# Kernel optimization log

Hardware: AMD Instinct MI355X
Metric: run time of the kernel (lower is better)

The kernel has to match this reference:

```python
import jax, jax.numpy as jnp
import numpy as np

B, T, D, M = 8, 4096, 64, 1024  # batch, frames, embedding_dim, codebook size


def setup_inputs() -> dict:
    key = jax.random.key(0)
    k1, k2, k3 = jax.random.split(key, 3)
    x = jax.random.normal(k1, (B, D, T), dtype=jnp.float32)          # (B, channels=D, T)
    embedding = jax.random.normal(k2, (M, D), dtype=jnp.float32)     # codebook
    # Precomputed Gumbel noise, matching torch: -log(-log(clamp(U, eps, 1-eps)))
    eps = jnp.finfo(jnp.float32).eps
    u = jax.random.uniform(k3, (B * T, M), dtype=jnp.float32)
    gumbels = -jnp.log(-jnp.log(jnp.clip(u, eps, 1.0 - eps)))
    log_var_q = jnp.float32(0.0)
    temperature = jnp.float32(0.5)
    return {"x": x, "embedding": embedding, "log_var_q": log_var_q,
            "gumbels": gumbels, "temperature": temperature}


def reference(x, embedding, log_var_q, gumbels, temperature):
    B_, D_, T_ = x.shape
    M_ = embedding.shape[0]
    xt = jnp.swapaxes(x, 1, 2)                 # (B, T, D)
    x_flat = xt.reshape(-1, D_)                # (N, D)
    precision = jnp.exp(-log_var_q)            # scalar
    # 0.5 * precision * ||x - e||^2, via the GEMM expansion (fused cdist)
    sq = (jnp.sum(x_flat * x_flat, axis=1, keepdims=True)
          + jnp.sum(embedding * embedding, axis=1)[None, :]
          - 2.0 * x_flat @ embedding.T)        # (N, M)
    distances = 0.5 * precision * sq
    indices = jnp.argmin(distances, axis=-1)   # (N,)
    logits = -distances
    # gumbel-softmax (soft)
    encodings = jax.nn.softmax((logits + gumbels) / temperature, axis=-1)  # (N, M)
    quantized = (encodings @ embedding).reshape(B_, T_, D_)                # (B, T, D)
    logits3 = logits.reshape(B_, T_, M_)
    log_probs = jax.nn.log_softmax(logits3, axis=-1)
    probs = jnp.exp(log_probs)
    recon = 0.5 * precision * jnp.sum((xt - quantized) ** 2, axis=(1, 2))  # (B,)
    neg_entropy = jnp.sum(probs * log_probs, axis=(1, 2))                  # (B,)
    loss = jnp.mean(recon + neg_entropy)
    # perplexity over hard assignments
    one_hot = jax.nn.one_hot(indices, M_, dtype=jnp.float32)               # (N, M)
    avg_probs = jnp.mean(one_hot, axis=0)
    perplexity = jnp.exp(-jnp.sum(avg_probs * jnp.log(avg_probs + 1e-10)))
    return jnp.swapaxes(quantized, 1, 2), loss, perplexity
```

## Files before the change

### kernel.cpp

```cpp
#include <hip/hip_runtime.h>

#define T_DIM 4096
#define D_DIM 64
#define M_DIM 1024
#define N_ROWS 32768
#define TR 16
#define SC_STRIDE (M_DIM + 4)

typedef __attribute__((ext_vector_type(8))) short bf16x8;
typedef __attribute__((ext_vector_type(4))) float f32x4;

#define WS_BF16_OFF 4096

__device__ __forceinline__ short f2bfs(float f) {
  union { float f; unsigned u; } v; v.f = f;
  unsigned r = v.u + 0x7fffu + ((v.u >> 16) & 1u);
  return (short)(r >> 16);
}
__device__ __forceinline__ float bf2f(short h) {
  union { unsigned u; float f; } v; v.u = ((unsigned)(unsigned short)h) << 16;
  return v.f;
}
__device__ __forceinline__ void cvt8(const float* p, bf16x8& h8, bf16x8& l8) {
  float4 a = *(const float4*)p, b = *(const float4*)(p + 4);
  float v[8] = {a.x, a.y, a.z, a.w, b.x, b.y, b.z, b.w};
#pragma unroll
  for (int i = 0; i < 8; ++i) {
    short h = f2bfs(v[i]);
    h8[i] = h;
    l8[i] = f2bfs(v[i] - bf2f(h));
  }
}

__global__ void vq_conv(const float* __restrict__ emb, float* __restrict__ ws) {
  __shared__ short s_h[64][72], s_l[64][72];
  const int tid = threadIdx.x;
  const int mb = blockIdx.x * 64;
  short* EH = (short*)(ws + WS_BF16_OFF);
  short* EL = EH + 65536;
  short* ETH = EL + 65536;
  short* ETL = ETH + 65536;
#pragma unroll
  for (int i = 0; i < 16; ++i) {
    int lin = tid + 256 * i;
    int ml = lin >> 6, d = lin & 63;
    float v = emb[(size_t)(mb + ml) * 64 + d];
    short h = f2bfs(v);
    short l = f2bfs(v - bf2f(h));
    EH[(size_t)(mb + ml) * 64 + d] = h;
    EL[(size_t)(mb + ml) * 64 + d] = l;
    s_h[d][ml] = h;
    s_l[d][ml] = l;
  }
  if (tid < 64) {
    const float* e = emb + (size_t)(mb + tid) * 64;
    float s = 0.f;
#pragma unroll
    for (int d = 0; d < 64; d += 4) {
      float4 v = *(const float4*)(e + d);
      s += v.x * v.x + v.y * v.y + v.z * v.z + v.w * v.w;
    }
    ws[mb + tid] = s;
    ws[M_DIM + mb + tid] = 0.f;
  }
  if (blockIdx.x == 0 && tid == 0) ws[2 * M_DIM] = 0.f;
  __syncthreads();
#pragma unroll
  for (int i = 0; i < 16; ++i) {
    int lin = tid + 256 * i;
    int d = lin >> 6, ml = lin & 63;
    ETH[(size_t)d * 1024 + mb + ml] = s_h[d][ml];
    ETL[(size_t)d * 1024 + mb + ml] = s_l[d][ml];
  }
}

__global__ __launch_bounds__(256, 2) void vq_main(
    const float* __restrict__ x, const float* __restrict__ emb,
    const float* __restrict__ lvq, const float* __restrict__ gum,
    const float* __restrict__ temp, float* __restrict__ outq,
    float* __restrict__ ws) {
  __shared__ float s_sc[TR][SC_STRIDE];
  __shared__ float s_x[TR][68];
  __shared__ float s_xx[TR];
  __shared__ float s_red[4];

  const int tid = threadIdx.x;
  const int lane = tid & 63;
  const int wave = tid >> 6;
  const int mq = lane >> 4;
  const int mn = lane & 15;
  const int n0 = blockIdx.x * TR;
  const int b = n0 >> 12;
  const int t0 = n0 & (T_DIM - 1);
  const float precision = __expf(-lvq[0]);
  const float inv_temp = 1.0f / temp[0];
  const float* eew = ws;
  float* counts = ws + M_DIM;
  float* accum = ws + 2 * M_DIM;
  const short* EH = (const short*)(ws + WS_BF16_OFF);
  const short* EL = EH + 65536;
  const short* ETH = EL + 65536;
  const short* ETL = ETH + 65536;

  {
    int tt = tid & 15, d0 = tid >> 4;
#pragma unroll
    for (int k = 0; k < 4; ++k) {
      int d = d0 + 16 * k;
      s_x[tt][d] = x[((size_t)b << 18) + ((size_t)d << 12) + (size_t)(t0 + tt)];
    }
  }
  __syncthreads();
  if (tid < TR) {
    float s = 0.f;
#pragma unroll
    for (int d = 0; d < D_DIM; ++d) { float v = s_x[tid][d]; s += v * v; }
    s_xx[tid] = s;
  }
  __syncthreads();

  {
    bf16x8 ah0, al0, ah1, al1;
    cvt8(&s_x[mn][mq * 8], ah0, al0);
    cvt8(&s_x[mn][32 + mq * 8], ah1, al1);
    float xx4[4];
#pragma unroll
    for (int reg = 0; reg < 4; ++reg) xx4[reg] = s_xx[mq * 4 + reg];
    f32x4 acc[16];
#pragma unroll
    for (int tt = 0; tt < 16; ++tt) acc[tt] = (f32x4){0.f, 0.f, 0.f, 0.f};
#pragma unroll
    for (int tt = 0; tt < 16; ++tt) {
      int m0 = wave * 256 + tt * 16;
      const short* bp = EH + (m0 + mn) * 64 + mq * 8;
      const short* lp = EL + (m0 + mn) * 64 + mq * 8;
      bf16x8 bh0 = *(const bf16x8*)bp;
      bf16x8 bh1 = *(const bf16x8*)(bp + 32);
      bf16x8 bl0 = *(const bf16x8*)lp;
      bf16x8 bl1 = *(const bf16x8*)(lp + 32);
      acc[tt] = __builtin_amdgcn_mfma_f32_16x16x32_bf16(ah0, bh0, acc[tt], 0, 0, 0);
      acc[tt] = __builtin_amdgcn_mfma_f32_16x16x32_bf16(ah1, bh1, acc[tt], 0, 0, 0);
      acc[tt] = __builtin_amdgcn_mfma_f32_16x16x32_bf16(al0, bh0, acc[tt], 0, 0, 0);
      acc[tt] = __builtin_amdgcn_mfma_f32_16x16x32_bf16(al1, bh1, acc[tt], 0, 0, 0);
      acc[tt] = __builtin_amdgcn_mfma_f32_16x16x32_bf16(ah0, bl0, acc[tt], 0, 0, 0);
      acc[tt] = __builtin_amdgcn_mfma_f32_16x16x32_bf16(ah1, bl1, acc[tt], 0, 0, 0);
    }
#pragma unroll
    for (int tt = 0; tt < 16; ++tt) {
      int m0 = wave * 256 + tt * 16;
      float eev = eew[m0 + mn];
#pragma unroll
      for (int reg = 0; reg < 4; ++reg) {
        int r = mq * 4 + reg;
        s_sc[r][m0 + mn] = precision * (acc[tt][reg] - 0.5f * (xx4[reg] + eev));
      }
    }
  }
  __syncthreads();

  float partial = 0.f;

  for (int rr = 0; rr < 4; ++rr) {
    int r = wave * 4 + rr;
    int n = n0 + r;
    float s[16], g[16];
#pragma unroll
    for (int k = 0; k < 4; ++k) {
      float4 v = *(const float4*)&s_sc[r][4 * lane + 256 * k];
      s[4 * k + 0] = v.x; s[4 * k + 1] = v.y; s[4 * k + 2] = v.z; s[4 * k + 3] = v.w;
    }
    float mx = -1e30f; int mi = 0;
#pragma unroll
    for (int i = 0; i < 16; ++i) {
      int m = 4 * lane + 256 * (i >> 2) + (i & 3);
      if (s[i] > mx) { mx = s[i]; mi = m; }
    }
#pragma unroll
    for (int off = 32; off; off >>= 1) {
      float omx = __shfl_xor(mx, off);
      int omi = __shfl_xor(mi, off);
      if (omx > mx || (omx == mx && omi < mi)) { mx = omx; mi = omi; }
    }
    const float* gn = gum + ((size_t)n << 10);
#pragma unroll
    for (int k = 0; k < 4; ++k) {
      float4 v = *(const float4*)(gn + 4 * lane + 256 * k);
      g[4 * k + 0] = v.x; g[4 * k + 1] = v.y; g[4 * k + 2] = v.z; g[4 * k + 3] = v.w;
    }
    float gmx = -1e30f;
#pragma unroll
    for (int i = 0; i < 16; ++i) {
      float gv = (s[i] + g[i]) * inv_temp;
      g[i] = gv;
      gmx = fmaxf(gmx, gv);
    }
#pragma unroll
    for (int off = 32; off; off >>= 1) gmx = fmaxf(gmx, __shfl_xor(gmx, off));
    float Zs = 0.f, As = 0.f, Zg = 0.f;
#pragma unroll
    for (int i = 0; i < 16; ++i) {
      float a = s[i] - mx;
      float e = __expf(a);
      Zs += e; As += a * e;
      float eg = __expf(g[i] - gmx);
      g[i] = eg;
      Zg += eg;
    }
#pragma unroll
    for (int off = 32; off; off >>= 1) {
      Zs += __shfl_xor(Zs, off);
      As += __shfl_xor(As, off);
      Zg += __shfl_xor(Zg, off);
    }
    float invZg = 1.0f / Zg;
#pragma unroll
    for (int k = 0; k < 4; ++k) {
      float4 w;
      w.x = g[4 * k + 0] * invZg; w.y = g[4 * k + 1] * invZg;
      w.z = g[4 * k + 2] * invZg; w.w = g[4 * k + 3] * invZg;
      *(float4*)&s_sc[r][4 * lane + 256 * k] = w;
    }
    if (lane == 0) {
      partial += As / Zs - __logf(Zs);
      atomicAdd(counts + mi, 1.0f);
    }
  }
  __syncthreads();

  {
    f32x4 q[4];
#pragma unroll
    for (int nt = 0; nt < 4; ++nt) q[nt] = (f32x4){0.f, 0.f, 0.f, 0.f};
    int k0w = wave * 256;
#pragma unroll 2
    for (int ks = 0; ks < 8; ++ks) {
      int k0 = k0w + ks * 32;
      bf16x8 ph, pl;
      cvt8(&s_sc[mn][k0 + mq * 8], ph, pl);
#pragma unroll
      for (int nt = 0; nt < 4; ++nt) {
        const short* bp = ETH + (nt * 16 + mn) * 1024 + k0 + mq * 8;
        const short* lp = ETL + (nt * 16 + mn) * 1024 + k0 + mq * 8;
        bf16x8 bh = *(const bf16x8*)bp;
        bf16x8 bl = *(const bf16x8*)lp;
        q[nt] = __builtin_amdgcn_mfma_f32_16x16x32_bf16(ph, bh, q[nt], 0, 0, 0);
        q[nt] = __builtin_amdgcn_mfma_f32_16x16x32_bf16(pl, bh, q[nt], 0, 0, 0);
        q[nt] = __builtin_amdgcn_mfma_f32_16x16x32_bf16(ph, bl, q[nt], 0, 0, 0);
      }
    }
    __syncthreads();
    float* qp = &s_sc[0][0];
#pragma unroll
    for (int nt = 0; nt < 4; ++nt)
#pragma unroll
      for (int reg = 0; reg < 4; ++reg)
        qp[(wave * 16 + mq * 4 + reg) * 68 + nt * 16 + mn] = q[nt][reg];
  }
  __syncthreads();

  {
    int r = tid & 15, dq = tid >> 4;
    const float* qp = &s_sc[0][0];
    float4 qs = {0.f, 0.f, 0.f, 0.f};
#pragma unroll
    for (int w = 0; w < 4; ++w) {
      float4 v = *(const float4*)&qp[(w * 16 + r) * 68 + 4 * dq];
      qs.x += v.x; qs.y += v.y; qs.z += v.z; qs.w += v.w;
    }
    int t = t0 + r;
    float* ob = outq + ((size_t)b << 18) + (size_t)t;
    int d = 4 * dq;
    ob[(size_t)(d + 0) << 12] = qs.x;
    ob[(size_t)(d + 1) << 12] = qs.y;
    ob[(size_t)(d + 2) << 12] = qs.z;
    ob[(size_t)(d + 3) << 12] = qs.w;
    float4 xv = *(const float4*)&s_x[r][d];
    float dx0 = xv.x - qs.x, dx1 = xv.y - qs.y, dx2 = xv.z - qs.z, dx3 = xv.w - qs.w;
    partial += 0.5f * precision * (dx0 * dx0 + dx1 * dx1 + dx2 * dx2 + dx3 * dx3);
  }
#pragma unroll
  for (int off = 32; off; off >>= 1) partial += __shfl_xor(partial, off);
  if (lane == 0) s_red[wave] = partial;
  __syncthreads();
  if (tid == 0)
    atomicAdd(accum, s_red[0] + s_red[1] + s_red[2] + s_red[3]);
}

__global__ void vq_finalize(const float* __restrict__ ws, float* __restrict__ out) {
  __shared__ float red[4];
  int tid = threadIdx.x;
  float h = 0.f;
  for (int m = tid; m < M_DIM; m += 256) {
    float avg = ws[M_DIM + m] * (1.0f / 32768.0f);
    h += avg * __logf(avg + 1e-10f);
  }
#pragma unroll
  for (int off = 32; off; off >>= 1) h += __shfl_xor(h, off);
  int lane = tid & 63, wave = tid >> 6;
  if (lane == 0) red[wave] = h;
  __syncthreads();
  if (tid == 0) {
    out[0] = ws[2 * M_DIM] * 0.125f;
    out[1] = __expf(-(red[0] + red[1] + red[2] + red[3]));
  }
}

extern "C" void kernel_launch(void* const* d_in, const int* in_sizes, int n_in,
                              void* d_out, int out_size, void* d_ws, size_t ws_size,
                              hipStream_t stream) {
  const float* x = (const float*)d_in[0];
  const float* emb = (const float*)d_in[1];
  const float* lvq = (const float*)d_in[2];
  const float* gum = (const float*)d_in[3];
  const float* temp = (const float*)d_in[4];
  float* out = (float*)d_out;
  float* ws = (float*)d_ws;

  hipLaunchKernelGGL(vq_conv, dim3(16), dim3(256), 0, stream, emb, ws);
  hipLaunchKernelGGL(vq_main, dim3(N_ROWS / TR), dim3(256), 0, stream,
                     x, emb, lvq, gum, temp, out, ws);
  hipLaunchKernelGGL(vq_finalize, dim3(1), dim3(256), 0, stream, ws,
                     out + (size_t)2097152);
}
```

Before: 318.9 us.

## Keep distance scores in MFMA registers, drop the 64KB shared score tile

The distance scores now stay in the MFMA accumulator registers instead of being written to a 16x1028 float shared tile. Argmin, both softmaxes and the entropy terms are computed in place, and per-wave partials are combined through small shared arrays. Probabilities are staged through a small per-wave shared buffer to form the bf16 operands for the second GEMM. With shared memory cut from about 66KB to about 22KB, launch bounds rise to 4 blocks per CU. The cost is two extra block barriers, more register pressure from holding 64 accumulators live, and uncoalesced strided gumbel loads.

```diff
diff --git a/kernel.cpp b/kernel.cpp
--- a/kernel.cpp
+++ b/kernel.cpp
@@ -5,7 +5,7 @@
 #define M_DIM 1024
 #define N_ROWS 32768
 #define TR 16
-#define SC_STRIDE (M_DIM + 4)
+#define NT 256
 
 typedef __attribute__((ext_vector_type(8))) short bf16x8;
 typedef __attribute__((ext_vector_type(4))) float f32x4;
@@ -74,19 +74,23 @@
   }
 }
 
-__global__ __launch_bounds__(256, 2) void vq_main(
+__global__ __launch_bounds__(NT, 4) void vq_main(
     const float* __restrict__ x, const float* __restrict__ emb,
     const float* __restrict__ lvq, const float* __restrict__ gum,
     const float* __restrict__ temp, float* __restrict__ outq,
     float* __restrict__ ws) {
-  __shared__ float s_sc[TR][SC_STRIDE];
   __shared__ float s_x[TR][68];
   __shared__ float s_xx[TR];
+  __shared__ float s_qp[4][TR][68];
+  __shared__ float s_stA_m[4][TR];
+  __shared__ int   s_stA_i[4][TR];
+  __shared__ float s_stB[4][TR][3];
+  __shared__ float s_stC[4][TR];
   __shared__ float s_red[4];
 
   const int tid = threadIdx.x;
   const int lane = tid & 63;
-  const int wave = tid >> 6;
+  const int wl = tid >> 6;
   const int mq = lane >> 4;
   const int mn = lane & 15;
   const int n0 = blockIdx.x * TR;
@@ -119,19 +123,16 @@
   }
   __syncthreads();
 
+  f32x4 acc[16];
   {
     bf16x8 ah0, al0, ah1, al1;
     cvt8(&s_x[mn][mq * 8], ah0, al0);
     cvt8(&s_x[mn][32 + mq * 8], ah1, al1);
-    float xx4[4];
-#pragma unroll
-    for (int reg = 0; reg < 4; ++reg) xx4[reg] = s_xx[mq * 4 + reg];
-    f32x4 acc[16];
 #pragma unroll
     for (int tt = 0; tt < 16; ++tt) acc[tt] = (f32x4){0.f, 0.f, 0.f, 0.f};
 #pragma unroll
     for (int tt = 0; tt < 16; ++tt) {
-      int m0 = wave * 256 + tt * 16;
+      int m0 = wl * 256 + tt * 16;
       const short* bp = EH + (m0 + mn) * 64 + mq * 8;
       const short* lp = EL + (m0 + mn) * 64 + mq * 8;
       bf16x8 bh0 = *(const bf16x8*)bp;
@@ -145,98 +146,142 @@
       acc[tt] = __builtin_amdgcn_mfma_f32_16x16x32_bf16(ah0, bl0, acc[tt], 0, 0, 0);
       acc[tt] = __builtin_amdgcn_mfma_f32_16x16x32_bf16(ah1, bl1, acc[tt], 0, 0, 0);
     }
+    float xx4[4];
+#pragma unroll
+    for (int reg = 0; reg < 4; ++reg) xx4[reg] = s_xx[mq * 4 + reg];
 #pragma unroll
     for (int tt = 0; tt < 16; ++tt) {
-      int m0 = wave * 256 + tt * 16;
-      float eev = eew[m0 + mn];
-#pragma unroll
-      for (int reg = 0; reg < 4; ++reg) {
-        int r = mq * 4 + reg;
-        s_sc[r][m0 + mn] = precision * (acc[tt][reg] - 0.5f * (xx4[reg] + eev));
-      }
-    }
-  }
-  __syncthreads();
-
-  float partial = 0.f;
-
-  for (int rr = 0; rr < 4; ++rr) {
-    int r = wave * 4 + rr;
-    int n = n0 + r;
-    float s[16], g[16];
-#pragma unroll
-    for (int k = 0; k < 4; ++k) {
-      float4 v = *(const float4*)&s_sc[r][4 * lane + 256 * k];
-      s[4 * k + 0] = v.x; s[4 * k + 1] = v.y; s[4 * k + 2] = v.z; s[4 * k + 3] = v.w;
-    }
-    float mx = -1e30f; int mi = 0;
-#pragma unroll
-    for (int i = 0; i < 16; ++i) {
-      int m = 4 * lane + 256 * (i >> 2) + (i & 3);
-      if (s[i] > mx) { mx = s[i]; mi = m; }
-    }
-#pragma unroll
-    for (int off = 32; off; off >>= 1) {
+      float eev = eew[wl * 256 + tt * 16 + mn];
+#pragma unroll
+      for (int reg = 0; reg < 4; ++reg)
+        acc[tt][reg] = precision * (acc[tt][reg] - 0.5f * (xx4[reg] + eev));
+    }
+  }
+
+  float Mx[4]; int Mi[4];
+#pragma unroll
+  for (int reg = 0; reg < 4; ++reg) {
+    float mx = acc[0][reg]; int mi = wl * 256 + mn;
+#pragma unroll
+    for (int tt = 1; tt < 16; ++tt) {
+      float v = acc[tt][reg];
+      int m = wl * 256 + tt * 16 + mn;
+      if (v > mx) { mx = v; mi = m; }
+    }
+#pragma unroll
+    for (int off = 1; off <= 8; off <<= 1) {
       float omx = __shfl_xor(mx, off);
       int omi = __shfl_xor(mi, off);
       if (omx > mx || (omx == mx && omi < mi)) { mx = omx; mi = omi; }
     }
-    const float* gn = gum + ((size_t)n << 10);
-#pragma unroll
-    for (int k = 0; k < 4; ++k) {
-      float4 v = *(const float4*)(gn + 4 * lane + 256 * k);
-      g[4 * k + 0] = v.x; g[4 * k + 1] = v.y; g[4 * k + 2] = v.z; g[4 * k + 3] = v.w;
-    }
-    float gmx = -1e30f;
-#pragma unroll
-    for (int i = 0; i < 16; ++i) {
-      float gv = (s[i] + g[i]) * inv_temp;
-      g[i] = gv;
-      gmx = fmaxf(gmx, gv);
-    }
-#pragma unroll
-    for (int off = 32; off; off >>= 1) gmx = fmaxf(gmx, __shfl_xor(gmx, off));
-    float Zs = 0.f, As = 0.f, Zg = 0.f;
-#pragma unroll
-    for (int i = 0; i < 16; ++i) {
-      float a = s[i] - mx;
+    if (mn == 0) { s_stA_m[wl][mq * 4 + reg] = mx; s_stA_i[wl][mq * 4 + reg] = mi; }
+  }
+  __syncthreads();
+#pragma unroll
+  for (int reg = 0; reg < 4; ++reg) {
+    int token = mq * 4 + reg;
+    Mx[reg] = s_stA_m[0][token]; Mi[reg] = s_stA_i[0][token];
+#pragma unroll
+    for (int w = 1; w < 4; ++w) {
+      float m2 = s_stA_m[w][token]; int i2 = s_stA_i[w][token];
+      if (m2 > Mx[reg] || (m2 == Mx[reg] && i2 < Mi[reg])) { Mx[reg] = m2; Mi[reg] = i2; }
+    }
+  }
+  float partial = 0.f;
+  if (wl == 0 && mn == 0) {
+#pragma unroll
+    for (int reg = 0; reg < 4; ++reg) atomicAdd(counts + Mi[reg], 1.0f);
+  }
+
+  float Zs[4] = {0.f, 0.f, 0.f, 0.f}, As[4] = {0.f, 0.f, 0.f, 0.f}, Gm[4];
+#pragma unroll
+  for (int reg = 0; reg < 4; ++reg) {
+    const float* gp = gum + ((size_t)(n0 + mq * 4 + reg) << 10) + wl * 256 + mn;
+    float gm = -1e30f;
+#pragma unroll
+    for (int tt = 0; tt < 16; ++tt) {
+      float g = gp[tt * 16];
+      float s = acc[tt][reg];
+      float a = s - Mx[reg];
       float e = __expf(a);
-      Zs += e; As += a * e;
-      float eg = __expf(g[i] - gmx);
-      g[i] = eg;
-      Zg += eg;
-    }
-#pragma unroll
-    for (int off = 32; off; off >>= 1) {
-      Zs += __shfl_xor(Zs, off);
-      As += __shfl_xor(As, off);
-      Zg += __shfl_xor(Zg, off);
-    }
-    float invZg = 1.0f / Zg;
-#pragma unroll
-    for (int k = 0; k < 4; ++k) {
-      float4 w;
-      w.x = g[4 * k + 0] * invZg; w.y = g[4 * k + 1] * invZg;
-      w.z = g[4 * k + 2] * invZg; w.w = g[4 * k + 3] * invZg;
-      *(float4*)&s_sc[r][4 * lane + 256 * k] = w;
-    }
-    if (lane == 0) {
-      partial += As / Zs - __logf(Zs);
-      atomicAdd(counts + mi, 1.0f);
-    }
-  }
-  __syncthreads();
+      Zs[reg] += e; As[reg] += a * e;
+      float gv = (s + g) * inv_temp;
+      acc[tt][reg] = gv;
+      gm = fmaxf(gm, gv);
+    }
+    Gm[reg] = gm;
+  }
+#pragma unroll
+  for (int reg = 0; reg < 4; ++reg) {
+#pragma unroll
+    for (int off = 1; off <= 8; off <<= 1) {
+      Zs[reg] += __shfl_xor(Zs[reg], off);
+      As[reg] += __shfl_xor(As[reg], off);
+      Gm[reg] = fmaxf(Gm[reg], __shfl_xor(Gm[reg], off));
+    }
+    if (mn == 0) {
+      s_stB[wl][mq * 4 + reg][0] = Zs[reg];
+      s_stB[wl][mq * 4 + reg][1] = As[reg];
+      s_stB[wl][mq * 4 + reg][2] = Gm[reg];
+    }
+  }
+  __syncthreads();
+  float GM[4];
+#pragma unroll
+  for (int reg = 0; reg < 4; ++reg) {
+    int token = mq * 4 + reg;
+    float zs = 0.f, as = 0.f, gmax = -1e30f;
+#pragma unroll
+    for (int w = 0; w < 4; ++w) {
+      zs += s_stB[w][token][0];
+      as += s_stB[w][token][1];
+      gmax = fmaxf(gmax, s_stB[w][token][2]);
+    }
+    GM[reg] = gmax;
+    if (wl == 0 && mn == 0) partial += as / zs - __logf(zs);
+  }
+  float Zg[4] = {0.f, 0.f, 0.f, 0.f};
+#pragma unroll
+  for (int tt = 0; tt < 16; ++tt) {
+#pragma unroll
+    for (int reg = 0; reg < 4; ++reg) {
+      float p = __expf(acc[tt][reg] - GM[reg]);
+      acc[tt][reg] = p;
+      Zg[reg] += p;
+    }
+  }
+#pragma unroll
+  for (int reg = 0; reg < 4; ++reg) {
+#pragma unroll
+    for (int off = 1; off <= 8; off <<= 1) Zg[reg] += __shfl_xor(Zg[reg], off);
+    if (mn == 0) s_stC[wl][mq * 4 + reg] = Zg[reg];
+  }
+  __syncthreads();
+  float invZg[4];
+#pragma unroll
+  for (int reg = 0; reg < 4; ++reg) {
+    int token = mq * 4 + reg;
+    float z = 0.f;
+#pragma unroll
+    for (int w = 0; w < 4; ++w) z += s_stC[w][token];
+    invZg[reg] = 1.0f / z;
+  }
 
   {
     f32x4 q[4];
 #pragma unroll
     for (int nt = 0; nt < 4; ++nt) q[nt] = (f32x4){0.f, 0.f, 0.f, 0.f};
-    int k0w = wave * 256;
-#pragma unroll 2
+    float* sp = &s_qp[wl][0][0];
+#pragma unroll
     for (int ks = 0; ks < 8; ++ks) {
-      int k0 = k0w + ks * 32;
+#pragma unroll
+      for (int reg = 0; reg < 4; ++reg) {
+        sp[(mq * 4 + reg) * 36 + mn]      = acc[2 * ks][reg] * invZg[reg];
+        sp[(mq * 4 + reg) * 36 + 16 + mn] = acc[2 * ks + 1][reg] * invZg[reg];
+      }
       bf16x8 ph, pl;
-      cvt8(&s_sc[mn][k0 + mq * 8], ph, pl);
+      cvt8(&sp[mn * 36 + mq * 8], ph, pl);
+      int k0 = wl * 256 + ks * 32;
 #pragma unroll
       for (int nt = 0; nt < 4; ++nt) {
         const short* bp = ETH + (nt * 16 + mn) * 1024 + k0 + mq * 8;
@@ -248,23 +293,20 @@
         q[nt] = __builtin_amdgcn_mfma_f32_16x16x32_bf16(ph, bl, q[nt], 0, 0, 0);
       }
     }
-    __syncthreads();
-    float* qp = &s_sc[0][0];
 #pragma unroll
     for (int nt = 0; nt < 4; ++nt)
 #pragma unroll
       for (int reg = 0; reg < 4; ++reg)
-        qp[(wave * 16 + mq * 4 + reg) * 68 + nt * 16 + mn] = q[nt][reg];
+        s_qp[wl][mq * 4 + reg][nt * 16 + mn] = q[nt][reg];
   }
   __syncthreads();
 
   {
     int r = tid & 15, dq = tid >> 4;
-    const float* qp = &s_sc[0][0];
     float4 qs = {0.f, 0.f, 0.f, 0.f};
 #pragma unroll
     for (int w = 0; w < 4; ++w) {
-      float4 v = *(const float4*)&qp[(w * 16 + r) * 68 + 4 * dq];
+      float4 v = *(const float4*)&s_qp[w][r][4 * dq];
       qs.x += v.x; qs.y += v.y; qs.z += v.z; qs.w += v.w;
     }
     int t = t0 + r;
@@ -280,7 +322,7 @@
   }
 #pragma unroll
   for (int off = 32; off; off >>= 1) partial += __shfl_xor(partial, off);
-  if (lane == 0) s_red[wave] = partial;
+  if (lane == 0) s_red[wl] = partial;
   __syncthreads();
   if (tid == 0)
     atomicAdd(accum, s_red[0] + s_red[1] + s_red[2] + s_red[3]);
@@ -317,7 +359,7 @@
   float* ws = (float*)d_ws;
 
   hipLaunchKernelGGL(vq_conv, dim3(16), dim3(256), 0, stream, emb, ws);
-  hipLaunchKernelGGL(vq_main, dim3(N_ROWS / TR), dim3(256), 0, stream,
+  hipLaunchKernelGGL(vq_main, dim3(N_ROWS / TR), dim3(NT), 0, stream,
                      x, emb, lvq, gum, temp, out, ws);
   hipLaunchKernelGGL(vq_finalize, dim3(1), dim3(256), 0, stream, ws,
                      out + (size_t)2097152);
```

Result: slower. 335.2 us (+5.1%).
